# Kernel tuning notes

Measured on AMD Instinct MI355X. Metric: run time of the kernel, lower is better.

## Reference

```python
import jax, jax.numpy as jnp
import numpy as np
from jax.ops import segment_sum

GRID = 32        # cells per axis; offset grid is (GRID+1)^3
T = 48           # number of accepted MC topologies
N_PTS = 131072

# 12 cube edges: base (lower) corner offset and axis the edge runs along.
# e0..3: x/y edges of z=0 face, e4..7: same at z=1, e8..11: vertical z edges.
EDGE_BASE = np.array([[0,0,0],[1,0,0],[0,1,0],[0,0,0],
                      [0,0,1],[1,0,1],[0,1,1],[0,0,1],
                      [0,0,0],[1,0,0],[1,1,0],[0,1,0]], dtype=np.int32)
EDGE_AXIS = np.array([0,1,0,1, 0,1,0,1, 2,2,2,2], dtype=np.int32)
EDGE_DIR  = np.eye(3, dtype=np.float32)[EDGE_AXIS]          # [12,3] unit dirs


def _dot(u, v):
    return jnp.sum(u * v, axis=-1)


def _safe_div(n, d, eps=1e-12):
    return n / jnp.where(jnp.abs(d) > eps, d, eps)


def _point_tri_dist_sq(p, a, b, c):
    """Squared distance from p to triangle (a,b,c); Ericson closest-point
    algorithm with full vertex/edge/interior region clamping, vectorized.
    p broadcasts against a/b/c over leading dims; last dim is xyz."""
    ab = b - a; ac = c - a; ap = p - a
    d1 = _dot(ab, ap); d2 = _dot(ac, ap)
    bp = p - b; d3 = _dot(ab, bp); d4 = _dot(ac, bp)
    cp = p - c; d5 = _dot(ab, cp); d6 = _dot(ac, cp)
    vc = d1 * d4 - d3 * d2
    vb = d5 * d2 - d1 * d6
    va = d3 * d6 - d5 * d4
    v_ab = _safe_div(d1, d1 - d3)
    w_ac = _safe_div(d2, d2 - d6)
    w_bc = _safe_div(d4 - d3, (d4 - d3) + (d5 - d6))
    inv = _safe_div(jnp.ones_like(va), va + vb + vc)
    v_in = vb * inv; w_in = vc * inv
    q = a + ab * v_in[..., None] + ac * w_in[..., None]                      # interior
    q = jnp.where(((va <= 0) & ((d4 - d3) >= 0) & ((d5 - d6) >= 0))[..., None],
                  b + (c - b) * w_bc[..., None], q)                          # edge BC
    q = jnp.where(((vb <= 0) & (d2 >= 0) & (d6 <= 0))[..., None],
                  a + ac * w_ac[..., None], q)                               # edge AC
    q = jnp.where(((d6 >= 0) & (d5 <= d6))[..., None], c, q)                 # vertex C
    q = jnp.where(((vc <= 0) & (d1 >= 0) & (d3 <= 0))[..., None],
                  a + ab * v_ab[..., None], q)                               # edge AB
    q = jnp.where(((d3 >= 0) & (d4 <= d3))[..., None], b, q)                 # vertex B
    q = jnp.where(((d1 <= 0) & (d2 <= 0))[..., None], a, q)                  # vertex A
    diff = p - q
    return _dot(diff, diff)


def setup_inputs() -> dict:
    key = jax.random.key(0)
    k1, k2, k3 = jax.random.split(key, 3)
    offset = jax.random.uniform(k1, (3, GRID + 1, GRID + 1, GRID + 1), dtype=jnp.float32)
    points = jax.random.uniform(k2, (N_PTS, 3), dtype=jnp.float32) * GRID
    tri_table = jax.random.randint(k3, (T, 3, 3), 0, 12, dtype=jnp.int32)
    return {"offset": offset, "points": points, "tri_table": tri_table}


def reference(offset, points, tri_table):
    edge_base_i = jnp.asarray(EDGE_BASE)                 # [12,3] int
    edge_base_f = jnp.asarray(EDGE_BASE, dtype=offset.dtype)
    edge_dir = jnp.asarray(EDGE_DIR, dtype=offset.dtype)
    edge_axis = jnp.asarray(EDGE_AXIS)

    cell = jnp.clip(jnp.floor(points).astype(jnp.int32), 0, GRID - 1)   # [N,3]
    local = points - cell.astype(points.dtype)                          # [N,3] in [0,1)^3

    # grid index of each edge's base corner -> edge offset parameter t in [0,1]
    gidx = cell[:, None, :] + edge_base_i[None, :, :]                   # [N,12,3]
    t = offset[edge_axis[None, :], gidx[..., 0], gidx[..., 1], gidx[..., 2]]  # [N,12]
    verts = edge_base_f[None] + edge_dir[None] * t[..., None]           # [N,12,3] local coords

    tri = verts[:, tri_table]                                           # [N,T,3tri,3vert,3]
    a = tri[:, :, :, 0, :]; b = tri[:, :, :, 1, :]; c = tri[:, :, :, 2, :]
    p = local[:, None, None, :]                                         # [N,1,1,3]
    d2 = _point_tri_dist_sq(p, a, b, c)                                 # [N,T,3]
    d_min = jnp.min(d2, axis=-1)                                        # [N,T]

    cell_id = (cell[:, 0] * GRID + cell[:, 1]) * GRID + cell[:, 2]      # [N]
    distances_full = segment_sum(d_min, cell_id, num_segments=GRID ** 3)  # [GRID^3, T]
    return distances_full
```

## Files before the change

kernel.cpp:

```cpp
#include <hip/hip_runtime.h>

#define GRID 32
#define NT 48
#define BLK 256
#define SPLIT 16
#define PPB (BLK / SPLIT)

#define EDGE_PACK ( (0ULL<<0) | (9ULL<<5) | (2ULL<<10) | (8ULL<<15) | \
                    (4ULL<<20) | (13ULL<<25) | (6ULL<<30) | (12ULL<<35) | \
                    (16ULL<<40) | (17ULL<<45) | (19ULL<<50) | (18ULL<<55) )

__device__ __forceinline__ float safe_div(float n, float d) {
    float dd = (fabsf(d) > 1e-12f) ? d : 1e-12f;
    return n * __builtin_amdgcn_rcpf(dd);
}

__device__ float tri_dist_sq(float Apx, float Apy, float Apz,
                             float Bpx, float Bpy, float Bpz,
                             float Cpx, float Cpy, float Cpz) {
    float abx = Apx - Bpx, aby = Apy - Bpy, abz = Apz - Bpz;
    float acx = Apx - Cpx, acy = Apy - Cpy, acz = Apz - Cpz;
    float d1 = abx * Apx + aby * Apy + abz * Apz;
    float d2 = acx * Apx + acy * Apy + acz * Apz;
    float d3 = abx * Bpx + aby * Bpy + abz * Bpz;
    float d4 = acx * Bpx + acy * Bpy + acz * Bpz;
    float d5 = abx * Cpx + aby * Cpy + abz * Cpz;
    float d6 = acx * Cpx + acy * Cpy + acz * Cpz;
    float vc = d1 * d4 - d3 * d2;
    float vb = d5 * d2 - d1 * d6;
    float va = d3 * d6 - d5 * d4;
    float d43 = d4 - d3;
    float d56 = d5 - d6;
    float v_ab = safe_div(d1, d1 - d3);
    float w_ac = safe_div(d2, d2 - d6);
    float w_bc = safe_div(d43, d43 + d56);
    float inv  = safe_div(1.0f, va + vb + vc);
    float v_in = vb * inv;
    float w_in = vc * inv;
    float dx = Apx - abx * v_in - acx * w_in;
    float dy = Apy - aby * v_in - acy * w_in;
    float dz = Apz - abz * v_in - acz * w_in;
    if ((va <= 0.0f) && (d43 >= 0.0f) && (d56 >= 0.0f)) {
        dx = Bpx - (Bpx - Cpx) * w_bc;
        dy = Bpy - (Bpy - Cpy) * w_bc;
        dz = Bpz - (Bpz - Cpz) * w_bc;
    }
    if ((vb <= 0.0f) && (d2 >= 0.0f) && (d6 <= 0.0f)) {
        dx = Apx - acx * w_ac;
        dy = Apy - acy * w_ac;
        dz = Apz - acz * w_ac;
    }
    if ((d6 >= 0.0f) && (d5 <= d6)) { dx = Cpx; dy = Cpy; dz = Cpz; }
    if ((vc <= 0.0f) && (d1 >= 0.0f) && (d3 <= 0.0f)) {
        dx = Apx - abx * v_ab;
        dy = Apy - aby * v_ab;
        dz = Apz - abz * v_ab;
    }
    if ((d3 >= 0.0f) && (d4 <= d3)) { dx = Bpx; dy = Bpy; dz = Bpz; }
    if ((d1 <= 0.0f) && (d2 <= 0.0f)) { dx = Apx; dy = Apy; dz = Apz; }
    return dx * dx + dy * dy + dz * dz;
}

__global__ __launch_bounds__(BLK) void ptd_kernel(
    const float* __restrict__ offset,
    const float* __restrict__ points,
    const int*   __restrict__ tri_table,
    float*       __restrict__ out,
    int n)
{
    __shared__ float4 v_s[PPB * 13];
    __shared__ int t_tab[NT * 3];

    const int tid = threadIdx.x;
    const int g   = blockIdx.x * BLK + tid;
    const int pt  = g >> 4;
    const int grp = tid & 15;
    const int pl  = tid >> 4;
    const bool active = (pt < n);

    if (tid < NT * 3) {
        int i0 = tri_table[tid * 3 + 0];
        int i1 = tri_table[tid * 3 + 1];
        int i2 = tri_table[tid * 3 + 2];
        t_tab[tid] = i0 | (i1 << 8) | (i2 << 16);
    }

    int cx = 0, cy = 0, cz = 0;
    if (active) {
        float px = points[pt * 3 + 0];
        float py = points[pt * 3 + 1];
        float pz = points[pt * 3 + 2];
        cx = min(max((int)floorf(px), 0), GRID - 1);
        cy = min(max((int)floorf(py), 0), GRID - 1);
        cz = min(max((int)floorf(pz), 0), GRID - 1);
        if (grp < 12) {
            float lx = px - (float)cx;
            float ly = py - (float)cy;
            float lz = pz - (float)cz;
            unsigned nib = (unsigned)(EDGE_PACK >> (5 * grp)) & 31u;
            int gx = cx + (int)(nib & 1u);
            int gy = cy + (int)((nib >> 1) & 1u);
            int gz = cz + (int)((nib >> 2) & 1u);
            int ax = (int)(nib >> 3);
            float t = offset[((ax * 33 + gx) * 33 + gy) * 33 + gz];
            float vx = (ax == 0) ? t : (float)(nib & 1u);
            float vy = (ax == 1) ? t : (float)((nib >> 1) & 1u);
            float vz = (ax == 2) ? t : (float)((nib >> 2) & 1u);
            v_s[pl * 13 + grp] = make_float4(lx - vx, ly - vy, lz - vz, 0.0f);
        }
    }
    __syncthreads();

    if (!active) return;

    const float4* vrow = &v_s[pl * 13];
    float* outp = out + ((((cx * GRID) + cy) * GRID + cz) * NT);

#pragma unroll
    for (int r = 0; r < 3; r++) {
        const int t = grp * 3 + r;
        float dmin;
#pragma unroll
        for (int k = 0; k < 3; k++) {
            int packed = t_tab[t * 3 + k];
            float4 A = vrow[packed & 255];
            float4 B = vrow[(packed >> 8) & 255];
            float4 C = vrow[(packed >> 16) & 255];
            float d = tri_dist_sq(A.x, A.y, A.z, B.x, B.y, B.z, C.x, C.y, C.z);
            dmin = (k == 0) ? d : fminf(dmin, d);
        }
        atomicAdd(&outp[t], dmin);
    }
}

extern "C" void kernel_launch(void* const* d_in, const int* in_sizes, int n_in,
                              void* d_out, int out_size, void* d_ws, size_t ws_size,
                              hipStream_t stream) {
    const float* offset    = (const float*)d_in[0];
    const float* points    = (const float*)d_in[1];
    const int*   tri_table = (const int*)d_in[2];
    float* out = (float*)d_out;
    int n = in_sizes[1] / 3;

    hipMemsetAsync(d_out, 0, (size_t)out_size * sizeof(float), stream);

    long total = (long)n * SPLIT;
    int blocks = (int)((total + BLK - 1) / BLK);
    ptd_kernel<<<blocks, BLK, 0, stream>>>(offset, points, tri_table, out, n);
}
```

Measured before the change: 125.0 us.

## Compute triangle distances from precomputed per-point Gram matrix of edge vertices

Each point now gets a 12x12 Gram matrix of dot products between its relative edge-vertex vectors, computed cooperatively and stored in shared memory. The point-triangle distance is rewritten to use only six Gram entries, with branch-free region selection and a single reciprocal per triangle. This removes redundant per-triangle dot products and most of the divergent branches. In exchange it adds a second barrier, a larger shared-memory footprint, and possible changes in float rounding from the algebraic reformulation.

```diff
diff --git a/kernel.cpp b/kernel.cpp
--- a/kernel.cpp
+++ b/kernel.cpp
@@ -10,55 +10,43 @@
                     (4ULL<<20) | (13ULL<<25) | (6ULL<<30) | (12ULL<<35) | \
                     (16ULL<<40) | (17ULL<<45) | (19ULL<<50) | (18ULL<<55) )
 
-__device__ __forceinline__ float safe_div(float n, float d) {
-    float dd = (fabsf(d) > 1e-12f) ? d : 1e-12f;
-    return n * __builtin_amdgcn_rcpf(dd);
-}
-
-__device__ float tri_dist_sq(float Apx, float Apy, float Apz,
-                             float Bpx, float Bpy, float Bpz,
-                             float Cpx, float Cpy, float Cpz) {
-    float abx = Apx - Bpx, aby = Apy - Bpy, abz = Apz - Bpz;
-    float acx = Apx - Cpx, acy = Apy - Cpy, acz = Apz - Cpz;
-    float d1 = abx * Apx + aby * Apy + abz * Apz;
-    float d2 = acx * Apx + acy * Apy + acz * Apz;
-    float d3 = abx * Bpx + aby * Bpy + abz * Bpz;
-    float d4 = acx * Bpx + acy * Bpy + acz * Bpz;
-    float d5 = abx * Cpx + aby * Cpy + abz * Cpz;
-    float d6 = acx * Cpx + acy * Cpy + acz * Cpz;
+__device__ __forceinline__ float tri_dist_gram(float AA, float AB, float AC,
+                                               float BB, float BC, float CC) {
+    float d1 = AA - AB, d2 = AA - AC;
+    float d3 = AB - BB, d4 = AB - BC;
+    float d5 = AC - BC, d6 = AC - CC;
+    float d43 = BB - BC;
+    float d56 = CC - BC;
     float vc = d1 * d4 - d3 * d2;
     float vb = d5 * d2 - d1 * d6;
     float va = d3 * d6 - d5 * d4;
-    float d43 = d4 - d3;
-    float d56 = d5 - d6;
-    float v_ab = safe_div(d1, d1 - d3);
-    float w_ac = safe_div(d2, d2 - d6);
-    float w_bc = safe_div(d43, d43 + d56);
-    float inv  = safe_div(1.0f, va + vb + vc);
-    float v_in = vb * inv;
-    float w_in = vc * inv;
-    float dx = Apx - abx * v_in - acx * w_in;
-    float dy = Apy - aby * v_in - acy * w_in;
-    float dz = Apz - abz * v_in - acz * w_in;
-    if ((va <= 0.0f) && (d43 >= 0.0f) && (d56 >= 0.0f)) {
-        dx = Bpx - (Bpx - Cpx) * w_bc;
-        dy = Bpy - (Bpy - Cpy) * w_bc;
-        dz = Bpz - (Bpz - Cpz) * w_bc;
-    }
-    if ((vb <= 0.0f) && (d2 >= 0.0f) && (d6 <= 0.0f)) {
-        dx = Apx - acx * w_ac;
-        dy = Apy - acy * w_ac;
-        dz = Apz - acz * w_ac;
-    }
-    if ((d6 >= 0.0f) && (d5 <= d6)) { dx = Cpx; dy = Cpy; dz = Cpz; }
-    if ((vc <= 0.0f) && (d1 >= 0.0f) && (d3 <= 0.0f)) {
-        dx = Apx - abx * v_ab;
-        dy = Apy - aby * v_ab;
-        dz = Apz - abz * v_ab;
-    }
-    if ((d3 >= 0.0f) && (d4 <= d3)) { dx = Bpx; dy = Bpy; dz = Bpz; }
-    if ((d1 <= 0.0f) && (d2 <= 0.0f)) { dx = Apx; dy = Apy; dz = Apz; }
-    return dx * dx + dy * dy + dz * dz;
+
+    bool cbc = (va <= 0.f) & (d43 >= 0.f) & (d56 >= 0.f);
+    bool cac = (vb <= 0.f) & (d2 >= 0.f) & (d6 <= 0.f);
+    bool ccc = (d6 >= 0.f) & (d5 <= d6);
+    bool cab = (vc <= 0.f) & (d1 >= 0.f) & (d3 <= 0.f);
+    bool cbb = (d3 >= 0.f) & (d4 <= d3);
+    bool caa = (d1 <= 0.f) & (d2 <= 0.f);
+
+    float nv = vb, nw = vc, den = va + vb + vc;
+    bool mode = false;
+    nw = cbc ? d43 : nw;  den = cbc ? d43 + d56 : den;  mode = cbc ? true  : mode;
+    nv = cac ? 0.f : nv;  nw = cac ? d2  : nw;  den = cac ? d2 - d6 : den;  mode = cac ? false : mode;
+    nw = ccc ? 1.f : nw;  den = ccc ? 1.f : den;  mode = ccc ? true  : mode;
+    nv = cab ? d1  : nv;  nw = cab ? 0.f : nw;  den = cab ? d1 - d3 : den;  mode = cab ? false : mode;
+    nw = cbb ? 0.f : nw;  den = cbb ? 1.f : den;  mode = cbb ? true  : mode;
+    nv = caa ? 0.f : nv;  nw = caa ? 0.f : nw;  den = caa ? 1.f : den;  mode = caa ? false : mode;
+
+    float dd  = (fabsf(den) > 1e-12f) ? den : 1e-12f;
+    float inv = __builtin_amdgcn_rcpf(dd);
+    float vp = nv * inv;
+    float wp = nw * inv;
+    float u = mode ? 0.f : 1.f - vp - wp;
+    float v = mode ? 1.f - wp : vp;
+    float e1 = fmaf(AC, wp, fmaf(AB, v, AA * u));
+    float e2 = fmaf(BC, wp, fmaf(BB, v, AB * u));
+    float e3 = fmaf(CC, wp, fmaf(BC, v, AC * u));
+    return fmaf(wp, e3, fmaf(v, e2, u * e1));
 }
 
 __global__ __launch_bounds__(BLK) void ptd_kernel(
@@ -69,7 +57,8 @@
     int n)
 {
     __shared__ float4 v_s[PPB * 13];
-    __shared__ int t_tab[NT * 3];
+    __shared__ float  gram[PPB * 144];
+    __shared__ int2   goff[NT * 3];
 
     const int tid = threadIdx.x;
     const int g   = blockIdx.x * BLK + tid;
@@ -79,12 +68,15 @@
     const bool active = (pt < n);
 
     if (tid < NT * 3) {
-        int i0 = tri_table[tid * 3 + 0];
-        int i1 = tri_table[tid * 3 + 1];
-        int i2 = tri_table[tid * 3 + 2];
-        t_tab[tid] = i0 | (i1 << 8) | (i2 << 16);
+        int i = tri_table[tid * 3 + 0];
+        int j = tri_table[tid * 3 + 1];
+        int k = tri_table[tid * 3 + 2];
+        int o0 = (i * 13) | ((i * 12 + j) << 8) | ((i * 12 + k) << 16);
+        int o1 = (j * 13) | ((j * 12 + k) << 8) | ((k * 13) << 16);
+        goff[tid] = make_int2(o0, o1);
     }
 
+    float4 vi = make_float4(0.f, 0.f, 0.f, 0.f);
     int cx = 0, cy = 0, cz = 0;
     if (active) {
         float px = points[pt * 3 + 0];
@@ -106,30 +98,48 @@
             float vx = (ax == 0) ? t : (float)(nib & 1u);
             float vy = (ax == 1) ? t : (float)((nib >> 1) & 1u);
             float vz = (ax == 2) ? t : (float)((nib >> 2) & 1u);
-            v_s[pl * 13 + grp] = make_float4(lx - vx, ly - vy, lz - vz, 0.0f);
+            vi = make_float4(lx - vx, ly - vy, lz - vz, 0.0f);
+            v_s[pl * 13 + grp] = vi;
+        }
+    }
+    __syncthreads();
+
+    if (active && grp < 12) {
+        float* gp = &gram[pl * 144];
+        int j = grp;
+#pragma unroll
+        for (int d = 0; d < 7; d++) {
+            float4 vj = v_s[pl * 13 + j];
+            float dv = fmaf(vi.z, vj.z, fmaf(vi.y, vj.y, vi.x * vj.x));
+            gp[grp * 12 + j] = dv;
+            gp[j * 12 + grp] = dv;
+            j = (j == 11) ? 0 : j + 1;
         }
     }
     __syncthreads();
 
     if (!active) return;
 
-    const float4* vrow = &v_s[pl * 13];
+    const float* gp = &gram[pl * 144];
     float* outp = out + ((((cx * GRID) + cy) * GRID + cz) * NT);
+    const int2* gofft = &goff[grp * 9];
 
 #pragma unroll
     for (int r = 0; r < 3; r++) {
-        const int t = grp * 3 + r;
         float dmin;
 #pragma unroll
         for (int k = 0; k < 3; k++) {
-            int packed = t_tab[t * 3 + k];
-            float4 A = vrow[packed & 255];
-            float4 B = vrow[(packed >> 8) & 255];
-            float4 C = vrow[(packed >> 16) & 255];
-            float d = tri_dist_sq(A.x, A.y, A.z, B.x, B.y, B.z, C.x, C.y, C.z);
+            int2 o = gofft[r * 3 + k];
+            float AA = gp[o.x & 255];
+            float AB = gp[(o.x >> 8) & 255];
+            float AC = gp[(unsigned)o.x >> 16];
+            float BB = gp[o.y & 255];
+            float BC = gp[(o.y >> 8) & 255];
+            float CC = gp[(unsigned)o.y >> 16];
+            float d = tri_dist_gram(AA, AB, AC, BB, BC, CC);
             dmin = (k == 0) ? d : fminf(dmin, d);
         }
-        atomicAdd(&outp[t], dmin);
+        atomicAdd(&outp[grp * 3 + r], dmin);
     }
 }
 
```

Result: no change. 127.1 us (+1.7%).
